# Performance work log

Measured on AMD Instinct MI355X. Metric: run time of the kernel, lower is better.

Reference implementation:

```python
import jax, jax.numpy as jnp
import numpy as np

ALPHA = 0.2  # LeakyReLU negative slope (self.alpha)
NEG_INF = -1e9


def setup_inputs() -> dict:
    key = jax.random.key(0)
    k1, k2, k3, k4, k5 = jax.random.split(key, 5)
    N, Fin, Fout = 8192, 256, 128
    return {
        "input": jax.random.normal(k1, (N, Fin), dtype=jnp.float32),
        "W": jax.random.normal(k2, (Fin, Fout), dtype=jnp.float32) * 0.1,
        "c1": jax.random.normal(k3, (Fout, 1), dtype=jnp.float32) * 0.1,
        "c2": jax.random.normal(k4, (Fout, 1), dtype=jnp.float32) * 0.1,
        "adj": jax.random.randint(k5, (N, N), 0, 2, dtype=jnp.int32),
        "M": N,
    }


def reference(input, W, c1, c2, adj, M):
    # h: [N, Fout]
    h = input @ W
    # valid neighbor j for row x: adj[x, j] > 0 and h[j].sum() != 0
    valid = (adj[:M] > 0) & (jnp.sum(h, axis=1) != 0.0)[None, :]  # [M, N]
    # e[x, j] = leakyrelu(h[x] @ c1 + h[j] @ c2)
    s_dst = (h[:M] @ c1)            # [M, 1]
    s_src = (h @ c2).T              # [1, N]
    e = jax.nn.leaky_relu(s_dst + s_src, negative_slope=ALPHA)
    e = jnp.where(valid, e, NEG_INF)
    attn = jax.nn.softmax(e, axis=1)
    attn = jnp.where(valid, attn, 0.0)  # rows with no neighbors -> all-zero weights
    # dropout is identity at inference (training=False); pool=0 branch skipped
    h_prime = attn @ h              # [M, Fout]
    return jax.nn.elu(h_prime)
```

## Files before the change

### kernel.cpp

```cpp
#include <hip/hip_runtime.h>
#include <math.h>

typedef __attribute__((ext_vector_type(8))) short bf16x8;
typedef __attribute__((ext_vector_type(4))) float f32x4;

#define GAT_ALPHA 0.2f
#define NS 8

static __device__ __forceinline__ unsigned short f2bf(float x) {
    unsigned u = __float_as_uint(x);
    u += 0x7fffu + ((u >> 16) & 1u);
    return (unsigned short)(u >> 16);
}
static __device__ __forceinline__ float bf2f(unsigned short b) {
    return __uint_as_float(((unsigned)b) << 16);
}

__global__ __launch_bounds__(512)
void k_prep(const float* __restrict__ input, const float* __restrict__ W,
            const float* __restrict__ c1, const float* __restrict__ c2,
            unsigned short* __restrict__ hb, float* __restrict__ ssx,
            float* __restrict__ sd, int N, int Fin, int Fout)
{
    __shared__ float in_lds[4][256];
    __shared__ float red[4][3];
    const int tid = threadIdx.x;
    const int r0 = blockIdx.x * 4;
    for (int idx = tid; idx < 4 * Fin; idx += 512) {
        int r = idx / Fin, c = idx - r * Fin;
        in_lds[r][c] = input[(size_t)(r0 + r) * Fin + c];
    }
    if (tid < 12) ((float*)red)[tid] = 0.f;
    __syncthreads();
    const int y = tid >> 7, f = tid & 127;
    float acc = 0.f;
    for (int k = 0; k < Fin; ++k)
        acc = fmaf(in_lds[y][k], W[(size_t)k * Fout + f], acc);
    const int row = r0 + y;
    hb[(size_t)row * Fout + f] = f2bf(acc);
    float rs = acc, sv = acc * c2[f], dv = acc * c1[f];
    for (int off = 32; off > 0; off >>= 1) {
        rs += __shfl_xor(rs, off);
        sv += __shfl_xor(sv, off);
        dv += __shfl_xor(dv, off);
    }
    if ((tid & 63) == 0) {
        atomicAdd(&red[y][0], rs);
        atomicAdd(&red[y][1], sv);
        atomicAdd(&red[y][2], dv);
    }
    __syncthreads();
    if (f == 0) {
        float rsum = red[y][0];
        ssx[row] = (rsum != 0.f) ? red[y][1] : -1e30f;
        sd[row]  = red[y][2];
    }
}

__global__ __launch_bounds__(1024)
void k_smax(const float* __restrict__ ssx, float* __restrict__ smax, int N)
{
    __shared__ float red[16];
    const int tid = threadIdx.x;
    float m = -3e38f;
    for (int i = tid; i < N; i += 1024) m = fmaxf(m, ssx[i]);
    for (int off = 32; off > 0; off >>= 1) m = fmaxf(m, __shfl_xor(m, off));
    if ((tid & 63) == 0) red[tid >> 6] = m;
    __syncthreads();
    if (tid == 0) {
        float mm = red[0];
        for (int i = 1; i < 16; ++i) mm = fmaxf(mm, red[i]);
        smax[0] = mm;
    }
}

__global__ __launch_bounds__(256)
void k_transpose(const unsigned short* __restrict__ hb, unsigned short* __restrict__ ht,
                 int N, int Fout)
{
    __shared__ unsigned short t[64][65];
    const int bx = blockIdx.x;
    const int by = blockIdx.y;
    const int tid = threadIdx.x;
    for (int i = 0; i < 16; ++i) {
        int idx = i * 256 + tid; int r = idx >> 6, c = idx & 63;
        t[r][c] = hb[(size_t)(bx * 64 + r) * Fout + by * 64 + c];
    }
    __syncthreads();
    for (int i = 0; i < 16; ++i) {
        int idx = i * 256 + tid; int r = idx >> 6, c = idx & 63;
        ht[(size_t)(by * 64 + r) * N + bx * 64 + c] = t[c][r];
    }
}

__global__ __launch_bounds__(512, 4)
void k_attn(const int* __restrict__ adj, const unsigned short* __restrict__ ht,
            const float* __restrict__ ssx, const float* __restrict__ sd,
            const float* __restrict__ smaxp, unsigned short* __restrict__ part,
            float* __restrict__ dpart, int N, int M)
{
    __shared__ char btile[65536];
    __shared__ float sxl[256];

    const int tid = threadIdx.x;
    const int w = tid >> 6, l = tid & 63, am = l & 15, kg = l >> 4, ams = am & 7;
    const int bi = blockIdx.x, bj = blockIdx.y;
    const int jch = N / NS;
    const int j0 = bj * jch;
    const int row = bi * 128 + w * 16 + am;

    const float s0 = sd[row];
    const float sm = smaxp[0];
    const float vb = s0 + sm;
    const float m0 = fmaxf(vb, GAT_ALPHA * vb);

    const int fb  = tid >> 5;
    const int pos = tid & 31;
    const int rbl = am * 512;

    const int* __restrict__ aptr = adj + (size_t)row * N + j0 + kg * 8;

    f32x4 acc[8];
    #pragma unroll
    for (int c = 0; c < 8; ++c) acc[c] = (f32x4){0.f, 0.f, 0.f, 0.f};
    float d0 = 0.f;

    int4 cA0 = *(const int4*)(aptr);
    int4 cA1 = *(const int4*)(aptr + 4);
    int4 cB0 = *(const int4*)(aptr + 32);
    int4 cB1 = *(const int4*)(aptr + 36);

    auto KS = [&](int q, int4& c0, int4& c1) {
        const int ks = q & 7;
        float4 x0 = *(const float4*)&sxl[ks * 32 + kg * 8];
        float4 x1 = *(const float4*)&sxl[ks * 32 + kg * 8 + 4];
        bf16x8 af;
        {
            unsigned short* pu = (unsigned short*)&af;
            const int* ai0 = (const int*)&c0;
            const int* ai1 = (const int*)&c1;
            const float* f0 = (const float*)&x0;
            const float* f1 = (const float*)&x1;
            float d = 0.f;
            #pragma unroll
            for (int i = 0; i < 4; ++i) {
                float v = s0 + f0[i];
                float e = fminf(fmaxf(v, GAT_ALPHA * v) - m0, 0.f);
                float p = (ai0[i] > 0) ? __expf(e) : 0.f;
                pu[i] = f2bf(p); d += p;
            }
            #pragma unroll
            for (int i = 0; i < 4; ++i) {
                float v = s0 + f1[i];
                float e = fminf(fmaxf(v, GAT_ALPHA * v) - m0, 0.f);
                float p = (ai1[i] > 0) ? __expf(e) : 0.f;
                pu[4 + i] = f2bf(p); d += p;
            }
            d0 += d;
        }
        const int qq = (q + 2 < 4 * 8) ? q + 2 : 4 * 8 - 1;
        c0 = *(const int4*)(aptr + qq * 32);
        c1 = *(const int4*)(aptr + qq * 32 + 4);
        const int sb = rbl + (((ks * 4 + kg) ^ ams) << 4);
        #pragma unroll
        for (int c = 0; c < 8; ++c) {
            bf16x8 bf = *(const bf16x8*)(btile + sb + c * 8192);
            acc[c] = __builtin_amdgcn_mfma_f32_16x16x32_bf16(af, bf, acc[c], 0, 0, 0);
        }
    };

    for (int ch = 0; ch < 4; ++ch) {
        if (ch) __syncthreads();
        #pragma unroll
        for (int it = 0; it < 8; ++it) {
            const int f = it * 16 + fb;
            bf16x8 v = *(const bf16x8*)(ht + (size_t)f * N + j0 + ch * 256 + pos * 8);
            *(bf16x8*)(btile + f * 512 + ((pos ^ (f & 7)) << 4)) = v;
        }
        if (tid < 64)
            *(float4*)&sxl[tid * 4] = *(const float4*)(ssx + j0 + ch * 256 + tid * 4);
        __syncthreads();
        #pragma unroll
        for (int ks = 0; ks < 8; ks += 2) {
            KS(ch * 8 + ks,     cA0, cA1);
            KS(ch * 8 + ks + 1, cB0, cB1);
        }
    }

    d0 += __shfl_xor(d0, 16);
    d0 += __shfl_xor(d0, 32);
    if (kg == 0) dpart[(size_t)bj * M + row] = d0;

    unsigned short* pb = part + (size_t)bj * M * 128
                       + ((((size_t)bi * 8 + w) * 64 + l) * 32);
    #pragma unroll
    for (int ec = 0; ec < 4; ++ec) {
        const f32x4 x = acc[ec * 2];
        const f32x4 y = acc[ec * 2 + 1];
        bf16x8 pv;
        unsigned short* pp = (unsigned short*)&pv;
        pp[0] = f2bf(x[0]); pp[1] = f2bf(x[1]); pp[2] = f2bf(x[2]); pp[3] = f2bf(x[3]);
        pp[4] = f2bf(y[0]); pp[5] = f2bf(y[1]); pp[6] = f2bf(y[2]); pp[7] = f2bf(y[3]);
        *(bf16x8*)(pb + ec * 8) = pv;
    }
}

__global__ __launch_bounds__(256)
void k_dsum(const float* __restrict__ dpart, float* __restrict__ denom, int M, int nsp)
{
    const int r = blockIdx.x * 256 + threadIdx.x;
    if (r < M) {
        float d = 0.f;
        for (int s = 0; s < nsp; ++s) d += dpart[(size_t)s * M + r];
        denom[r] = d;
    }
}

__global__ __launch_bounds__(256)
void k_combine(const unsigned short* __restrict__ part, const float* __restrict__ denom,
               float* __restrict__ out, int M, int nsp)
{
    const int idx = blockIdx.x * 256 + threadIdx.x;
    const int rbk = idx >> 11;
    const int rem = idx & 2047;
    const int w  = rem >> 8;
    const int l  = (rem >> 2) & 63;
    const int ec = rem & 3;
    const int am = l & 15, kg = l >> 4;

    float sums[8] = {0.f, 0.f, 0.f, 0.f, 0.f, 0.f, 0.f, 0.f};
    const unsigned short* p = part + (size_t)idx * 8;
    for (int s = 0; s < nsp; ++s) {
        bf16x8 v = *(const bf16x8*)(p + (size_t)s * M * 128);
        const unsigned short* vp = (const unsigned short*)&v;
        #pragma unroll
        for (int i = 0; i < 8; ++i) sums[i] += bf2f(vp[i]);
    }
    const int rbase = rbk * 128 + w * 16 + kg * 4;
    #pragma unroll
    for (int reg = 0; reg < 4; ++reg) {
        const float dd = denom[rbase + reg];
        const float inv = (dd > 0.f) ? 1.f / dd : 0.f;
        #pragma unroll
        for (int half = 0; half < 2; ++half) {
            float x = sums[half * 4 + reg] * inv;
            x = (x > 0.f) ? x : expm1f(x);
            out[(size_t)(rbase + reg) * 128 + (ec * 2 + half) * 16 + am] = x;
        }
    }
}

extern "C" void kernel_launch(void* const* d_in, const int* in_sizes, int n_in,
                              void* d_out, int out_size, void* d_ws, size_t ws_size,
                              hipStream_t stream)
{
    const float* input = (const float*)d_in[0];
    const float* W     = (const float*)d_in[1];
    const float* c1    = (const float*)d_in[2];
    const float* c2    = (const float*)d_in[3];
    const int*   adj   = (const int*)d_in[4];

    const int Fout = in_sizes[2];
    const int Fin  = in_sizes[1] / Fout;
    const int N    = in_sizes[0] / Fin;
    const int M    = out_size / Fout;
    float* out = (float*)d_out;

    char* ws = (char*)d_ws;
    const size_t o_hb   = 0;
    const size_t o_ht   = o_hb + (size_t)N * Fout * 2;
    const size_t o_ssx  = o_ht + (size_t)N * Fout * 2;
    const size_t o_sd   = o_ssx + (size_t)N * 4;
    const size_t o_smax = o_sd + (size_t)N * 4;
    const size_t o_den  = o_smax + 64;
    const size_t o_dpart = o_den + (((size_t)M * 4 + 63) & ~63ULL);
    const size_t o_part = (o_dpart + (size_t)NS * M * 4 + 63) & ~63ULL;

    unsigned short* hb = (unsigned short*)(ws + o_hb);
    unsigned short* ht = (unsigned short*)(ws + o_ht);
    float* ssx   = (float*)(ws + o_ssx);
    float* sd    = (float*)(ws + o_sd);
    float* smax  = (float*)(ws + o_smax);
    float* denom = (float*)(ws + o_den);
    float* dpart = (float*)(ws + o_dpart);
    unsigned short* part = (unsigned short*)(ws + o_part);

    k_prep<<<N / 4, 512, 0, stream>>>(input, W, c1, c2, hb, ssx, sd, N, Fin, Fout);
    k_smax<<<1, 1024, 0, stream>>>(ssx, smax, N);
    k_transpose<<<dim3(N / 64, Fout / 64), 256, 0, stream>>>(hb, ht, N, Fout);

    k_attn<<<dim3(M / 128, NS), 512, 0, stream>>>(
        adj, ht, ssx, sd, smax, part, dpart, N, M);

    k_dsum<<<(M + 255) / 256, 256, 0, stream>>>(dpart, denom, M, NS);
    k_combine<<<M * Fout / 8 / 256, 256, 0, stream>>>(part, denom, out, M, NS);
}
```

Before: 150.0 us.

## Pack adjacency into bitmask and restage attention kernel with wider split

Adds a pre-pass that compresses the int32 adjacency matrix into a bitmask with wave ballots. The attention kernel then reads compact bits staged in LDS instead of streaming full int32 adjacency rows. The kernel also uses smaller 128-column feature chunks in dynamic shared memory and picks a split count up to 16 based on workspace size. The full adjacency read still happens once in the pack kernel, plus an extra launch and a bitmask write. A larger split count also means more partial results for the combine step to sum.

```diff
diff --git a/kernel.cpp b/kernel.cpp
--- a/kernel.cpp
+++ b/kernel.cpp
@@ -5,7 +5,6 @@
 typedef __attribute__((ext_vector_type(4))) float f32x4;
 
 #define GAT_ALPHA 0.2f
-#define NS 8
 
 static __device__ __forceinline__ unsigned short f2bf(float x) {
     unsigned u = __float_as_uint(x);
@@ -14,6 +13,24 @@
 }
 static __device__ __forceinline__ float bf2f(unsigned short b) {
     return __uint_as_float(((unsigned)b) << 16);
+}
+
+__global__ __launch_bounds__(256)
+void k_pack(const int* __restrict__ adj, unsigned long long* __restrict__ bits, int N)
+{
+    const int wid  = (blockIdx.x * 256 + threadIdx.x) >> 6;
+    const int lane = threadIdx.x & 63;
+    const int wpr  = N >> 6;
+    const int* __restrict__ ap = adj + (size_t)wid * N + lane;
+    unsigned long long* __restrict__ op = bits + (size_t)wid * wpr;
+    for (int k = 0; k < wpr; k += 8) {
+        #pragma unroll
+        for (int u = 0; u < 8; ++u) {
+            int v = ap[(k + u) * 64];
+            unsigned long long m = __ballot(v > 0);
+            if (lane == 0) op[k + u] = m;
+        }
+    }
 }
 
 __global__ __launch_bounds__(512)
@@ -94,18 +111,20 @@
 }
 
 __global__ __launch_bounds__(512, 4)
-void k_attn(const int* __restrict__ adj, const unsigned short* __restrict__ ht,
+void k_attn(const unsigned* __restrict__ packed, const unsigned short* __restrict__ ht,
             const float* __restrict__ ssx, const float* __restrict__ sd,
             const float* __restrict__ smaxp, unsigned short* __restrict__ part,
-            float* __restrict__ dpart, int N, int M)
-{
-    __shared__ char btile[65536];
-    __shared__ float sxl[256];
+            float* __restrict__ dpart, int N, int M, int jch)
+{
+    extern __shared__ char smem[];
+    char* btile = smem;
+    unsigned* bits = (unsigned*)(smem + 32768);
+    const int wpr = jch >> 5;
+    float* sxl = (float*)(smem + 32768 + 128 * wpr * 4);
 
     const int tid = threadIdx.x;
-    const int w = tid >> 6, l = tid & 63, am = l & 15, kg = l >> 4, ams = am & 7;
+    const int w = tid >> 6, l = tid & 63, am = l & 15, kg = l >> 4;
     const int bi = blockIdx.x, bj = blockIdx.y;
-    const int jch = N / NS;
     const int j0 = bj * jch;
     const int row = bi * 128 + w * 16 + am;
 
@@ -114,76 +133,84 @@
     const float vb = s0 + sm;
     const float m0 = fmaxf(vb, GAT_ALPHA * vb);
 
-    const int fb  = tid >> 5;
-    const int pos = tid & 31;
-    const int rbl = am * 512;
-
-    const int* __restrict__ aptr = adj + (size_t)row * N + j0 + kg * 8;
+    {
+        const int gwpr = N >> 5;
+        const int wsh  = 31 - __clz(wpr);
+        const int total = 128 << wsh;
+        for (int idx = tid; idx < total; idx += 512) {
+            const int r = idx >> wsh;
+            const int q = idx & (wpr - 1);
+            bits[r * wpr + (q ^ (r & (wpr - 1)))] =
+                packed[(size_t)(bi * 128 + r) * gwpr + (j0 >> 5) + q];
+        }
+        for (int idx = tid; idx * 4 < jch; idx += 512)
+            *(float4*)&sxl[idx * 4] = *(const float4*)(ssx + j0 + idx * 4);
+    }
+
+    const int fst = tid >> 2;
+    const int sub = tid & 3;
+    const unsigned short* __restrict__ gst = ht + (size_t)fst * N + j0 + sub * 32;
+    const int fsw = fst & 15;
 
     f32x4 acc[8];
     #pragma unroll
     for (int c = 0; c < 8; ++c) acc[c] = (f32x4){0.f, 0.f, 0.f, 0.f};
     float d0 = 0.f;
 
-    int4 cA0 = *(const int4*)(aptr);
-    int4 cA1 = *(const int4*)(aptr + 4);
-    int4 cB0 = *(const int4*)(aptr + 32);
-    int4 cB1 = *(const int4*)(aptr + 36);
-
-    auto KS = [&](int q, int4& c0, int4& c1) {
-        const int ks = q & 7;
-        float4 x0 = *(const float4*)&sxl[ks * 32 + kg * 8];
-        float4 x1 = *(const float4*)&sxl[ks * 32 + kg * 8 + 4];
-        bf16x8 af;
+    const int rl = w * 16 + am;
+    const unsigned* __restrict__ brow = bits + rl * wpr;
+    const int bswz = rl & (wpr - 1);
+
+    const int nch = jch >> 7;
+    for (int ch = 0; ch < nch; ++ch) {
+        if (ch) __syncthreads();
         {
-            unsigned short* pu = (unsigned short*)&af;
-            const int* ai0 = (const int*)&c0;
-            const int* ai1 = (const int*)&c1;
-            const float* f0 = (const float*)&x0;
-            const float* f1 = (const float*)&x1;
-            float d = 0.f;
-            #pragma unroll
-            for (int i = 0; i < 4; ++i) {
-                float v = s0 + f0[i];
-                float e = fminf(fmaxf(v, GAT_ALPHA * v) - m0, 0.f);
-                float p = (ai0[i] > 0) ? __expf(e) : 0.f;
-                pu[i] = f2bf(p); d += p;
+            const unsigned short* g = gst + ch * 128;
+            bf16x8 v0 = *(const bf16x8*)(g);
+            bf16x8 v1 = *(const bf16x8*)(g + 8);
+            bf16x8 v2 = *(const bf16x8*)(g + 16);
+            bf16x8 v3 = *(const bf16x8*)(g + 24);
+            char* bt = btile + fst * 256;
+            *(bf16x8*)(bt + (((sub * 4 + 0) ^ fsw) << 4)) = v0;
+            *(bf16x8*)(bt + (((sub * 4 + 1) ^ fsw) << 4)) = v1;
+            *(bf16x8*)(bt + (((sub * 4 + 2) ^ fsw) << 4)) = v2;
+            *(bf16x8*)(bt + (((sub * 4 + 3) ^ fsw) << 4)) = v3;
+        }
+        __syncthreads();
+        #pragma unroll
+        for (int ks = 0; ks < 4; ++ks) {
+            const int q = ch * 4 + ks;
+            const unsigned bb = brow[q ^ bswz] >> (8 * kg);
+            float4 x0 = *(const float4*)&sxl[q * 32 + kg * 8];
+            float4 x1 = *(const float4*)&sxl[q * 32 + kg * 8 + 4];
+            bf16x8 af;
+            {
+                unsigned short* pu = (unsigned short*)&af;
+                const float* f0 = (const float*)&x0;
+                const float* f1 = (const float*)&x1;
+                float dd = 0.f;
+                #pragma unroll
+                for (int i = 0; i < 4; ++i) {
+                    float v = s0 + f0[i];
+                    float e = fminf(fmaxf(v, GAT_ALPHA * v) - m0, 0.f);
+                    float p = (bb & (1u << i)) ? __expf(e) : 0.f;
+                    pu[i] = f2bf(p); dd += p;
+                }
+                #pragma unroll
+                for (int i = 0; i < 4; ++i) {
+                    float v = s0 + f1[i];
+                    float e = fminf(fmaxf(v, GAT_ALPHA * v) - m0, 0.f);
+                    float p = (bb & (16u << i)) ? __expf(e) : 0.f;
+                    pu[4 + i] = f2bf(p); dd += p;
+                }
+                d0 += dd;
             }
             #pragma unroll
-            for (int i = 0; i < 4; ++i) {
-                float v = s0 + f1[i];
-                float e = fminf(fmaxf(v, GAT_ALPHA * v) - m0, 0.f);
-                float p = (ai1[i] > 0) ? __expf(e) : 0.f;
-                pu[4 + i] = f2bf(p); d += p;
+            for (int c = 0; c < 8; ++c) {
+                bf16x8 bf = *(const bf16x8*)(btile + (c * 16 + am) * 256
+                                             + (((ks * 4 + kg) ^ am) << 4));
+                acc[c] = __builtin_amdgcn_mfma_f32_16x16x32_bf16(af, bf, acc[c], 0, 0, 0);
             }
-            d0 += d;
-        }
-        const int qq = (q + 2 < 4 * 8) ? q + 2 : 4 * 8 - 1;
-        c0 = *(const int4*)(aptr + qq * 32);
-        c1 = *(const int4*)(aptr + qq * 32 + 4);
-        const int sb = rbl + (((ks * 4 + kg) ^ ams) << 4);
-        #pragma unroll
-        for (int c = 0; c < 8; ++c) {
-            bf16x8 bf = *(const bf16x8*)(btile + sb + c * 8192);
-            acc[c] = __builtin_amdgcn_mfma_f32_16x16x32_bf16(af, bf, acc[c], 0, 0, 0);
-        }
-    };
-
-    for (int ch = 0; ch < 4; ++ch) {
-        if (ch) __syncthreads();
-        #pragma unroll
-        for (int it = 0; it < 8; ++it) {
-            const int f = it * 16 + fb;
-            bf16x8 v = *(const bf16x8*)(ht + (size_t)f * N + j0 + ch * 256 + pos * 8);
-            *(bf16x8*)(btile + f * 512 + ((pos ^ (f & 7)) << 4)) = v;
-        }
-        if (tid < 64)
-            *(float4*)&sxl[tid * 4] = *(const float4*)(ssx + j0 + ch * 256 + tid * 4);
-        __syncthreads();
-        #pragma unroll
-        for (int ks = 0; ks < 8; ks += 2) {
-            KS(ch * 8 + ks,     cA0, cA1);
-            KS(ch * 8 + ks + 1, cB0, cB1);
         }
     }
 
@@ -273,8 +300,18 @@
     const size_t o_sd   = o_ssx + (size_t)N * 4;
     const size_t o_smax = o_sd + (size_t)N * 4;
     const size_t o_den  = o_smax + 64;
-    const size_t o_dpart = o_den + (((size_t)M * 4 + 63) & ~63ULL);
-    const size_t o_part = (o_dpart + (size_t)NS * M * 4 + 63) & ~63ULL;
+    const size_t o_bits = (o_den + (size_t)M * 4 + 63) & ~63ULL;
+    const size_t bits_b = (size_t)N * N / 8;
+    const size_t o_dpart = (o_bits + bits_b + 63) & ~63ULL;
+
+    int NS = 16;
+    size_t o_part = 0;
+    while (NS >= 1) {
+        size_t op = (o_dpart + (size_t)NS * M * 4 + 63) & ~63ULL;
+        if (op + (size_t)NS * M * Fout * 2 <= ws_size) { o_part = op; break; }
+        NS >>= 1;
+    }
+    const int jch = N / NS;
 
     unsigned short* hb = (unsigned short*)(ws + o_hb);
     unsigned short* ht = (unsigned short*)(ws + o_ht);
@@ -282,15 +319,18 @@
     float* sd    = (float*)(ws + o_sd);
     float* smax  = (float*)(ws + o_smax);
     float* denom = (float*)(ws + o_den);
+    unsigned long long* bits = (unsigned long long*)(ws + o_bits);
     float* dpart = (float*)(ws + o_dpart);
     unsigned short* part = (unsigned short*)(ws + o_part);
 
+    k_pack<<<N / 4, 256, 0, stream>>>(adj, bits, N);
     k_prep<<<N / 4, 512, 0, stream>>>(input, W, c1, c2, hb, ssx, sd, N, Fin, Fout);
     k_smax<<<1, 1024, 0, stream>>>(ssx, smax, N);
     k_transpose<<<dim3(N / 64, Fout / 64), 256, 0, stream>>>(hb, ht, N, Fout);
 
-    k_attn<<<dim3(M / 128, NS), 512, 0, stream>>>(
-        adj, ht, ssx, sd, smax, part, dpart, N, M);
+    const size_t smem_bytes = 32768 + (size_t)128 * (jch >> 5) * 4 + (size_t)jch * 4;
+    k_attn<<<dim3(M / 128, NS), 512, smem_bytes, stream>>>(
+        (const unsigned*)bits, ht, ssx, sd, smax, part, dpart, N, M, jch);
 
     k_dsum<<<(M + 255) / 256, 256, 0, stream>>>(dpart, denom, M, NS);
     k_combine<<<M * Fout / 8 / 256, 256, 0, stream>>>(part, denom, out, M, NS);
```

Measured after the change: 199.3 us. 32.9% more time.

## Pack adjacency into LDS bitmasks and switch attention to 32x32 MFMA tiles

Applied to the files above, without the earlier changes.

The attention kernel now first streams each block's slice of the int32 adjacency matrix into a swizzled LDS bitmask, instead of keeping per-lane int4 prefetches interleaved with the MFMA loop. It uses 256-thread blocks with 32x32x16 bf16 MFMAs, four 16-wide accumulators, and a smaller 32KB B tile. The j-dimension split is raised to 16 when the workspace is large enough, and the combine kernel's index mapping is updated for the new partial-output layout. The intent is better MFMA efficiency and decoupling the adjacency loads from compute. The cost is more partial-sum traffic for the combine step and an up-front adjacency phase with no overlap against compute.

```diff
diff --git a/kernel.cpp b/kernel.cpp
--- a/kernel.cpp
+++ b/kernel.cpp
@@ -2,10 +2,9 @@
 #include <math.h>
 
 typedef __attribute__((ext_vector_type(8))) short bf16x8;
-typedef __attribute__((ext_vector_type(4))) float f32x4;
+typedef __attribute__((ext_vector_type(16))) float f32x16;
 
 #define GAT_ALPHA 0.2f
-#define NS 8
 
 static __device__ __forceinline__ unsigned short f2bf(float x) {
     unsigned u = __float_as_uint(x);
@@ -93,116 +92,147 @@
     }
 }
 
-__global__ __launch_bounds__(512, 4)
+template<int JCH>
+__global__ __launch_bounds__(256, 3)
 void k_attn(const int* __restrict__ adj, const unsigned short* __restrict__ ht,
             const float* __restrict__ ssx, const float* __restrict__ sd,
             const float* __restrict__ smaxp, unsigned short* __restrict__ part,
             float* __restrict__ dpart, int N, int M)
 {
-    __shared__ char btile[65536];
-    __shared__ float sxl[256];
+    constexpr int WPR = JCH / 32;
+    constexpr int NCH = JCH / 128;
+    __shared__ unsigned bits[128 * WPR];
+    __shared__ float sxl[JCH];
+    __shared__ char btile[32768];
 
     const int tid = threadIdx.x;
-    const int w = tid >> 6, l = tid & 63, am = l & 15, kg = l >> 4, ams = am & 7;
     const int bi = blockIdx.x, bj = blockIdx.y;
-    const int jch = N / NS;
-    const int j0 = bj * jch;
-    const int row = bi * 128 + w * 16 + am;
-
+    const int rb = bi * 128;
+    const int j0 = bj * JCH;
+
+    for (int i = tid * 4; i < JCH; i += 1024)
+        *(float4*)&sxl[i] = *(const float4*)(ssx + j0 + i);
+
+    {
+        const int w4 = tid >> 6, lane = tid & 63;
+        constexpr int IPASS = JCH / 512;
+        unsigned char* bb8 = (unsigned char*)bits;
+        for (int it = 0; it < 32; ++it) {
+            const int r = it * 4 + w4;
+            #pragma unroll
+            for (int ps = 0; ps < IPASS; ++ps) {
+                const int* __restrict__ ap =
+                    adj + (size_t)(rb + r) * N + j0 + ps * 512 + lane * 8;
+                int4 v0 = *(const int4*)ap;
+                int4 v1 = *(const int4*)(ap + 4);
+                unsigned b = (unsigned)(v0.x > 0)       | ((unsigned)(v0.y > 0) << 1)
+                           | ((unsigned)(v0.z > 0) << 2) | ((unsigned)(v0.w > 0) << 3)
+                           | ((unsigned)(v1.x > 0) << 4) | ((unsigned)(v1.y > 0) << 5)
+                           | ((unsigned)(v1.z > 0) << 6) | ((unsigned)(v1.w > 0) << 7);
+                const int wq = ps * 16 + (lane >> 2);
+                bb8[r * (WPR * 4) + ((wq ^ (r & (WPR - 1))) << 2) + (lane & 3)] =
+                    (unsigned char)b;
+            }
+        }
+    }
+
+    const int w = tid >> 6, l = tid & 63;
+    const int col = l & 31, hi = l >> 5;
+    const int rl = w * 32 + col;
+    const int row = rb + rl;
     const float s0 = sd[row];
-    const float sm = smaxp[0];
-    const float vb = s0 + sm;
+    const float vb = s0 + smaxp[0];
     const float m0 = fmaxf(vb, GAT_ALPHA * vb);
 
-    const int fb  = tid >> 5;
-    const int pos = tid & 31;
-    const int rbl = am * 512;
-
-    const int* __restrict__ aptr = adj + (size_t)row * N + j0 + kg * 8;
-
-    f32x4 acc[8];
-    #pragma unroll
-    for (int c = 0; c < 8; ++c) acc[c] = (f32x4){0.f, 0.f, 0.f, 0.f};
+    const int fst = tid >> 1, hpart = tid & 1;
+    const unsigned short* __restrict__ gst = ht + (size_t)fst * N + j0 + hpart * 64;
+    char* const wbase = btile + fst * 256;
+    const int fsw = fst & 7;
+
+    const unsigned* __restrict__ brow = bits + rl * WPR;
+    const int bswz = rl & (WPR - 1);
+    const int soffbase = col & 7;
+
+    f32x16 acc0 = {0,0,0,0,0,0,0,0,0,0,0,0,0,0,0,0};
+    f32x16 acc1 = {0,0,0,0,0,0,0,0,0,0,0,0,0,0,0,0};
+    f32x16 acc2 = {0,0,0,0,0,0,0,0,0,0,0,0,0,0,0,0};
+    f32x16 acc3 = {0,0,0,0,0,0,0,0,0,0,0,0,0,0,0,0};
     float d0 = 0.f;
 
-    int4 cA0 = *(const int4*)(aptr);
-    int4 cA1 = *(const int4*)(aptr + 4);
-    int4 cB0 = *(const int4*)(aptr + 32);
-    int4 cB1 = *(const int4*)(aptr + 36);
-
-    auto KS = [&](int q, int4& c0, int4& c1) {
-        const int ks = q & 7;
-        float4 x0 = *(const float4*)&sxl[ks * 32 + kg * 8];
-        float4 x1 = *(const float4*)&sxl[ks * 32 + kg * 8 + 4];
-        bf16x8 af;
-        {
-            unsigned short* pu = (unsigned short*)&af;
-            const int* ai0 = (const int*)&c0;
-            const int* ai1 = (const int*)&c1;
-            const float* f0 = (const float*)&x0;
-            const float* f1 = (const float*)&x1;
-            float d = 0.f;
-            #pragma unroll
-            for (int i = 0; i < 4; ++i) {
-                float v = s0 + f0[i];
-                float e = fminf(fmaxf(v, GAT_ALPHA * v) - m0, 0.f);
-                float p = (ai0[i] > 0) ? __expf(e) : 0.f;
-                pu[i] = f2bf(p); d += p;
-            }
-            #pragma unroll
-            for (int i = 0; i < 4; ++i) {
-                float v = s0 + f1[i];
-                float e = fminf(fmaxf(v, GAT_ALPHA * v) - m0, 0.f);
-                float p = (ai1[i] > 0) ? __expf(e) : 0.f;
-                pu[4 + i] = f2bf(p); d += p;
-            }
-            d0 += d;
-        }
-        const int qq = (q + 2 < 4 * 8) ? q + 2 : 4 * 8 - 1;
-        c0 = *(const int4*)(aptr + qq * 32);
-        c1 = *(const int4*)(aptr + qq * 32 + 4);
-        const int sb = rbl + (((ks * 4 + kg) ^ ams) << 4);
-        #pragma unroll
-        for (int c = 0; c < 8; ++c) {
-            bf16x8 bf = *(const bf16x8*)(btile + sb + c * 8192);
-            acc[c] = __builtin_amdgcn_mfma_f32_16x16x32_bf16(af, bf, acc[c], 0, 0, 0);
-        }
-    };
-
-    for (int ch = 0; ch < 4; ++ch) {
+    __syncthreads();
+
+    for (int ch = 0; ch < NCH; ++ch) {
         if (ch) __syncthreads();
         #pragma unroll
-        for (int it = 0; it < 8; ++it) {
-            const int f = it * 16 + fb;
-            bf16x8 v = *(const bf16x8*)(ht + (size_t)f * N + j0 + ch * 256 + pos * 8);
-            *(bf16x8*)(btile + f * 512 + ((pos ^ (f & 7)) << 4)) = v;
+        for (int s = 0; s < 8; ++s) {
+            bf16x8 v = *(const bf16x8*)(gst + ch * 128 + s * 8);
+            *(bf16x8*)(wbase + (((hpart * 8 + s) ^ fsw) << 4)) = v;
         }
-        if (tid < 64)
-            *(float4*)&sxl[tid * 4] = *(const float4*)(ssx + j0 + ch * 256 + tid * 4);
         __syncthreads();
         #pragma unroll
-        for (int ks = 0; ks < 8; ks += 2) {
-            KS(ch * 8 + ks,     cA0, cA1);
-            KS(ch * 8 + ks + 1, cB0, cB1);
+        for (int ks = 0; ks < 8; ++ks) {
+            const unsigned bb = brow[(ch * 4 + (ks >> 1)) ^ bswz]
+                                >> ((ks & 1) * 16 + hi * 8);
+            const float* sx = &sxl[ch * 128 + ks * 16 + hi * 8];
+            float4 x0 = *(const float4*)sx;
+            float4 x1 = *(const float4*)(sx + 4);
+            bf16x8 af;
+            {
+                unsigned short* pu = (unsigned short*)&af;
+                const float* f0 = (const float*)&x0;
+                const float* f1 = (const float*)&x1;
+                float dd = 0.f;
+                #pragma unroll
+                for (int i = 0; i < 4; ++i) {
+                    float v = s0 + f0[i];
+                    float a = fmaxf(v, GAT_ALPHA * v);
+                    float e = fminf(a - m0, 0.f);
+                    float p = (bb & (1u << i)) ? __expf(e) : 0.f;
+                    pu[i] = f2bf(p); dd += p;
+                }
+                #pragma unroll
+                for (int i = 0; i < 4; ++i) {
+                    float v = s0 + f1[i];
+                    float a = fmaxf(v, GAT_ALPHA * v);
+                    float e = fminf(a - m0, 0.f);
+                    float p = (bb & (16u << i)) ? __expf(e) : 0.f;
+                    pu[4 + i] = f2bf(p); dd += p;
+                }
+                d0 += dd;
+            }
+            const int soff = ((ks * 2 + hi) ^ soffbase) << 4;
+            const char* bp = btile + col * 256 + soff;
+            bf16x8 b0 = *(const bf16x8*)(bp);
+            bf16x8 b1 = *(const bf16x8*)(bp + 8192);
+            bf16x8 b2 = *(const bf16x8*)(bp + 16384);
+            bf16x8 b3 = *(const bf16x8*)(bp + 24576);
+            acc0 = __builtin_amdgcn_mfma_f32_32x32x16_bf16(af, b0, acc0, 0, 0, 0);
+            acc1 = __builtin_amdgcn_mfma_f32_32x32x16_bf16(af, b1, acc1, 0, 0, 0);
+            acc2 = __builtin_amdgcn_mfma_f32_32x32x16_bf16(af, b2, acc2, 0, 0, 0);
+            acc3 = __builtin_amdgcn_mfma_f32_32x32x16_bf16(af, b3, acc3, 0, 0, 0);
         }
     }
 
-    d0 += __shfl_xor(d0, 16);
     d0 += __shfl_xor(d0, 32);
-    if (kg == 0) dpart[(size_t)bj * M + row] = d0;
+    if (hi == 0) dpart[(size_t)bj * M + row] = d0;
 
     unsigned short* pb = part + (size_t)bj * M * 128
-                       + ((((size_t)bi * 8 + w) * 64 + l) * 32);
-    #pragma unroll
-    for (int ec = 0; ec < 4; ++ec) {
-        const f32x4 x = acc[ec * 2];
-        const f32x4 y = acc[ec * 2 + 1];
-        bf16x8 pv;
-        unsigned short* pp = (unsigned short*)&pv;
-        pp[0] = f2bf(x[0]); pp[1] = f2bf(x[1]); pp[2] = f2bf(x[2]); pp[3] = f2bf(x[3]);
-        pp[4] = f2bf(y[0]); pp[5] = f2bf(y[1]); pp[6] = f2bf(y[2]); pp[7] = f2bf(y[3]);
-        *(bf16x8*)(pb + ec * 8) = pv;
-    }
+                       + (((size_t)(bi * 4 + w) * 256) + l) * 16;
+    #define STORE_TILE(A, t) { \
+        bf16x8 lo, hic; \
+        unsigned short* q0 = (unsigned short*)&lo; \
+        unsigned short* q1 = (unsigned short*)&hic; \
+        q0[0]=f2bf(A[0]); q0[1]=f2bf(A[1]); q0[2]=f2bf(A[2]); q0[3]=f2bf(A[3]); \
+        q0[4]=f2bf(A[4]); q0[5]=f2bf(A[5]); q0[6]=f2bf(A[6]); q0[7]=f2bf(A[7]); \
+        q1[0]=f2bf(A[8]); q1[1]=f2bf(A[9]); q1[2]=f2bf(A[10]); q1[3]=f2bf(A[11]); \
+        q1[4]=f2bf(A[12]); q1[5]=f2bf(A[13]); q1[6]=f2bf(A[14]); q1[7]=f2bf(A[15]); \
+        *(bf16x8*)(pb + (size_t)(t) * 1024) = lo; \
+        *(bf16x8*)(pb + (size_t)(t) * 1024 + 8) = hic; }
+    STORE_TILE(acc0, 0)
+    STORE_TILE(acc1, 1)
+    STORE_TILE(acc2, 2)
+    STORE_TILE(acc3, 3)
+    #undef STORE_TILE
 }
 
 __global__ __launch_bounds__(256)
@@ -221,12 +251,13 @@
                float* __restrict__ out, int M, int nsp)
 {
     const int idx = blockIdx.x * 256 + threadIdx.x;
-    const int rbk = idx >> 11;
-    const int rem = idx & 2047;
-    const int w  = rem >> 8;
-    const int l  = (rem >> 2) & 63;
-    const int ec = rem & 3;
-    const int am = l & 15, kg = l >> 4;
+    const int s8 = idx & 1;
+    const int l  = (idx >> 1) & 63;
+    const int t  = (idx >> 7) & 3;
+    const int w  = (idx >> 9) & 3;
+    const int bi = idx >> 11;
+    const int colg = t * 32 + (l & 31);
+    const int hi = l >> 5;
 
     float sums[8] = {0.f, 0.f, 0.f, 0.f, 0.f, 0.f, 0.f, 0.f};
     const unsigned short* p = part + (size_t)idx * 8;
@@ -236,17 +267,16 @@
         #pragma unroll
         for (int i = 0; i < 8; ++i) sums[i] += bf2f(vp[i]);
     }
-    const int rbase = rbk * 128 + w * 16 + kg * 4;
+    const int rbase = bi * 128 + w * 32 + 4 * hi;
     #pragma unroll
-    for (int reg = 0; reg < 4; ++reg) {
-        const float dd = denom[rbase + reg];
+    for (int i = 0; i < 8; ++i) {
+        const int reg = s8 * 8 + i;
+        const int row = rbase + (reg & 3) + 8 * (reg >> 2);
+        const float dd = denom[row];
         const float inv = (dd > 0.f) ? 1.f / dd : 0.f;
-        #pragma unroll
-        for (int half = 0; half < 2; ++half) {
-            float x = sums[half * 4 + reg] * inv;
-            x = (x > 0.f) ? x : expm1f(x);
-            out[(size_t)(rbase + reg) * 128 + (ec * 2 + half) * 16 + am] = x;
-        }
+        float x = sums[i] * inv;
+        x = (x > 0.f) ? x : expm1f(x);
+        out[(size_t)row * 128 + colg] = x;
     }
 }
 
@@ -273,7 +303,13 @@
     const size_t o_sd   = o_ssx + (size_t)N * 4;
     const size_t o_smax = o_sd + (size_t)N * 4;
     const size_t o_den  = o_smax + 64;
-    const size_t o_dpart = o_den + (((size_t)M * 4 + 63) & ~63ULL);
+    const size_t o_dpart = (o_den + (size_t)M * 4 + 63) & ~63ULL;
+
+    int NS = 16;
+    {
+        size_t op16 = (o_dpart + (size_t)16 * M * 4 + 63) & ~63ULL;
+        if (op16 + (size_t)16 * M * Fout * 2 > ws_size) NS = 8;
+    }
     const size_t o_part = (o_dpart + (size_t)NS * M * 4 + 63) & ~63ULL;
 
     unsigned short* hb = (unsigned short*)(ws + o_hb);
@@ -289,8 +325,12 @@
     k_smax<<<1, 1024, 0, stream>>>(ssx, smax, N);
     k_transpose<<<dim3(N / 64, Fout / 64), 256, 0, stream>>>(hb, ht, N, Fout);
 
-    k_attn<<<dim3(M / 128, NS), 512, 0, stream>>>(
-        adj, ht, ssx, sd, smax, part, dpart, N, M);
+    if (NS == 16)
+        k_attn<512><<<dim3(M / 128, 16), 256, 0, stream>>>(
+            adj, ht, ssx, sd, smax, part, dpart, N, M);
+    else
+        k_attn<1024><<<dim3(M / 128, 8), 256, 0, stream>>>(
+            adj, ht, ssx, sd, smax, part, dpart, N, M);
 
     k_dsum<<<(M + 255) / 256, 256, 0, stream>>>(dpart, denom, M, NS);
     k_combine<<<M * Fout / 8 / 256, 256, 0, stream>>>(part, denom, out, M, NS);
```

Measured after the change: 159.1 us. 6.1% more time.
